# Kernel optimization log

Hardware: AMD Instinct MI355X
Metric: run time of the kernel (lower is better)

## Reference

```python
import jax, jax.numpy as jnp
import numpy as np

B, IN, E, NCLS = 1024, 784, 256, 10
BRAIN, ADIM, NJUMPS = 4, 3, 4
N = BRAIN ** ADIM  # 64 blocks
TAU = 1.0
_GKEY = jax.random.key(42)  # fixed key -> deterministic gumbel noise


def _gumbel_softmax_hard(key, logits):
    u = jax.random.uniform(key, logits.shape, minval=1e-6, maxval=1.0 - 1e-6)
    g = -jnp.log(-jnp.log(u))
    y = jax.nn.softmax((logits + g) / TAU, axis=-1)
    hard = jax.nn.one_hot(jnp.argmax(y, axis=-1), logits.shape[-1], dtype=y.dtype)
    return jax.lax.stop_gradient(hard - y) + y  # straight-through


def _next_address(state, key, at0_W1, at0_b1, at0_W2, at0_b2):
    # always uses block 0's address_transform (as in the original forward)
    h = jax.nn.relu(state @ at0_W1 + at0_b1)
    logits = (h @ at0_W2 + at0_b2).reshape(state.shape[0], ADIM, BRAIN)
    return _gumbel_softmax_hard(key, logits)  # (B, ADIM, BRAIN) one-hot


def _all_blocks(state, st_W1, st_b1, st_W2, st_b2):
    # state: (B,E); st_W*: (N,E,E) stored (in,out). Two batched GEMMs over all N blocks.
    h = jax.nn.relu(jnp.einsum('be,neh->bnh', state, st_W1) + st_b1[None])
    h = jax.nn.relu(jnp.einsum('bnh,nhg->bng', h, st_W2) + st_b2[None])
    norm = jnp.linalg.norm(state, axis=1, keepdims=True)  # (B,1), norm of INPUT state
    return h / (norm[:, :, None] + 1e-6)  # (B,N,E)


def _flatten_onehot(oh):
    # (B, ADIM, BRAIN) -> (B, BRAIN**ADIM) via iterated outer product
    b = oh.shape[0]
    fw = oh[:, 0, :]
    for d in range(1, oh.shape[1]):
        fw = (fw[:, :, None] * oh[:, d, None, :]).reshape(b, -1)
    return fw


def _forward(x, W_emb, b_emb, st_W1, st_b1, st_W2, st_b2,
             at0_W1, at0_b1, at0_W2, at0_b2, out_W1, out_b1, out_W2, out_b2):
    bsz = x.shape[0]
    state = x.reshape(bsz, -1) @ W_emb + b_emb
    initial_state = state
    current_address = _next_address(state, jax.random.fold_in(_GKEY, 0),
                                    at0_W1, at0_b1, at0_W2, at0_b2)
    exited = jnp.zeros((bsz,), dtype=bool)
    exit_states = jnp.zeros_like(state)
    exit_addresses = jnp.zeros_like(current_address)
    for i in range(NJUMPS):  # fixed small jump count; early-break replaced by masking (same math)
        active = ~exited
        bw = _flatten_onehot(current_address)                      # (B,N)
        allout = _all_blocks(state, st_W1, st_b1, st_W2, st_b2)    # (B,N,E)
        new_state = jnp.einsum('bn,bne->be', bw, allout)
        new_address = _next_address(new_state, jax.random.fold_in(_GKEY, i + 1),
                                    at0_W1, at0_b1, at0_W2, at0_b2)
        idx = jnp.argmax(new_address, axis=2)
        is_origin = jnp.all(idx == 0, axis=1) & active
        exit_states = jnp.where(is_origin[:, None], new_state, exit_states)
        exit_addresses = jnp.where(is_origin[:, None, None], new_address, exit_addresses)
        exited = exited | is_origin
        state = jnp.where(active[:, None], new_state, state)
        current_address = jnp.where(active[:, None, None], new_address, current_address)
    final_address = jnp.where(exited[:, None, None], exit_addresses, current_address)
    bw = _flatten_onehot(final_address)
    # original code computes block_out twice and keeps the one using `state` (bug-faithful)
    allout = _all_blocks(state, st_W1, st_b1, st_W2, st_b2)
    final_output = jnp.einsum('bn,bne->be', bw, allout) + initial_state
    h = jax.nn.relu(final_output @ out_W1 + out_b1)
    return h @ out_W2 + out_b2  # (B, NCLS)


def setup_inputs() -> dict:
    key = jax.random.key(0)
    ks = jax.random.split(key, 16)
    s = 0.02
    return {
        'x': jax.random.normal(ks[0], (B, IN), jnp.float32),
        'W_emb': jax.random.normal(ks[1], (IN, E), jnp.float32) * s,
        'b_emb': jnp.zeros((E,), jnp.float32),
        'st_W1': jax.random.normal(ks[2], (N, E, E), jnp.float32) * s,
        'st_b1': jnp.zeros((N, E), jnp.float32),
        'st_W2': jax.random.normal(ks[3], (N, E, E), jnp.float32) * s,
        'st_b2': jnp.zeros((N, E), jnp.float32),
        'at0_W1': jax.random.normal(ks[4], (E, E), jnp.float32) * s,
        'at0_b1': jnp.zeros((E,), jnp.float32),
        'at0_W2': jax.random.normal(ks[5], (E, ADIM * BRAIN), jnp.float32) * s,
        'at0_b2': jnp.zeros((ADIM * BRAIN,), jnp.float32),
        'out_W1': jax.random.normal(ks[6], (E, E), jnp.float32) * s,
        'out_b1': jnp.zeros((E,), jnp.float32),
        'out_W2': jax.random.normal(ks[7], (E, NCLS), jnp.float32) * s,
        'out_b2': jnp.zeros((NCLS,), jnp.float32),
    }


def reference(x, W_emb, b_emb, st_W1, st_b1, st_W2, st_b2,
              at0_W1, at0_b1, at0_W2, at0_b2, out_W1, out_b1, out_W2, out_b2):
    return _forward(x, W_emb, b_emb, st_W1, st_b1, st_W2, st_b2,
                    at0_W1, at0_b1, at0_W2, at0_b2, out_W1, out_b1, out_W2, out_b2)
```

## Files before the change

kernel.cpp:

```cpp
#include <hip/hip_runtime.h>
#include <stdint.h>


#define BATCH 1024
#define EDIM  256
#define INDIM 784
#define GRID_BE 192

__host__ __device__ inline uint32_t rotl32(uint32_t x, uint32_t d) {
  return (x << d) | (x >> (32u - d));
}
__host__ __device__ inline void threefry2x32(uint32_t k0, uint32_t k1,
                                             uint32_t x0, uint32_t x1,
                                             uint32_t* o0, uint32_t* o1) {
  uint32_t ks2 = k0 ^ k1 ^ 0x1BD11BDAu;
  x0 += k0; x1 += k1;
#define TF_R(a) { x0 += x1; x1 = rotl32(x1, a); x1 ^= x0; }
  TF_R(13) TF_R(15) TF_R(26) TF_R(6)   x0 += k1;  x1 += ks2 + 1u;
  TF_R(17) TF_R(29) TF_R(16) TF_R(24)  x0 += ks2; x1 += k0  + 2u;
  TF_R(13) TF_R(15) TF_R(26) TF_R(6)   x0 += k0;  x1 += k1  + 3u;
  TF_R(17) TF_R(29) TF_R(16) TF_R(24)  x0 += k1;  x1 += ks2 + 4u;
  TF_R(13) TF_R(15) TF_R(26) TF_R(6)   x0 += ks2; x1 += k0  + 5u;
#undef TF_R
  *o0 = x0; *o1 = x1;
}
__device__ inline uint32_t jax_bits12288(uint32_t k0, uint32_t k1, uint32_t L) {
  uint32_t o0, o1;
  if (L < 6144u) { threefry2x32(k0, k1, L, L + 6144u, &o0, &o1); return o0; }
  else           { threefry2x32(k0, k1, L - 6144u, L, &o0, &o1); return o1; }
}
__device__ inline float jax_uniform(uint32_t bits) {
  const float minv = 1e-6f;
  const float maxv = (float)(1.0 - 1e-06);
  const float span = maxv - minv;
  uint32_t fb = (bits >> 9) | 0x3f800000u;
  float f = __uint_as_float(fb) - 1.0f;
  float u = __fadd_rn(__fmul_rn(f, span), minv);
  return fmaxf(minv, u);
}

__global__ __launch_bounds__(1024) void k_embed(
    const float* __restrict__ x, const float* __restrict__ Wemb,
    const float* __restrict__ bemb,
    float* __restrict__ stateA, float* __restrict__ initial,
    int* __restrict__ count0) {
  __shared__ float XS[8 * INDIM];
  __shared__ float P[8][128][9];
  const int t = threadIdx.x;
  if (blockIdx.x == 0 && t < 64) count0[t] = 0;
  const int rg = blockIdx.x >> 1, ch = blockIdx.x & 1;
  const int jl = t & 127, ks = t >> 7;

  {
    const float4* src = (const float4*)(x + (size_t)rg * 8 * INDIM);
    float4* dst = (float4*)XS;
    for (int p = t; p < (8 * INDIM) / 4; p += 1024) dst[p] = src[p];
  }
  __syncthreads();

  const int col = ch * 128 + jl;
  const int kb = (ks < 4) ? ks * 100 : 400 + (ks - 4) * 96;
  const int ke = kb + ((ks < 4) ? 100 : 96);
  float a[8] = {0.f,0.f,0.f,0.f,0.f,0.f,0.f,0.f};
#pragma unroll 2
  for (int k = kb; k < ke; k += 4) {
    const float w0 = Wemb[(k+0)*EDIM + col], w1 = Wemb[(k+1)*EDIM + col],
                w2 = Wemb[(k+2)*EDIM + col], w3 = Wemb[(k+3)*EDIM + col];
#pragma unroll
    for (int i = 0; i < 8; i++) {
      const float4 s4 = *(const float4*)&XS[i * INDIM + k];
      a[i] = fmaf(s4.x, w0, a[i]); a[i] = fmaf(s4.y, w1, a[i]);
      a[i] = fmaf(s4.z, w2, a[i]); a[i] = fmaf(s4.w, w3, a[i]);
    }
  }
#pragma unroll
  for (int q = 0; q < 8; q++) P[ks][jl][q] = a[q];
  __syncthreads();
  {
    const int c2 = t & 127, i = t >> 7;
    float s = 0.f;
#pragma unroll
    for (int w = 0; w < 8; w++) s += P[w][c2][i];
    s += bemb[ch * 128 + c2];
    const size_t idx = (size_t)(rg * 8 + i) * EDIM + ch * 128 + c2;
    stateA[idx] = s; initial[idx] = s;
  }
}

__global__ __launch_bounds__(1024) void k_addr(
    const float* __restrict__ state,
    const float* __restrict__ aW1, const float* __restrict__ ab1,
    const float* __restrict__ aW2, const float* __restrict__ ab2,
    int* __restrict__ exited, int* __restrict__ n_next, int* __restrict__ count,
    float* __restrict__ sout, int step, uint32_t fk0, uint32_t fk1) {
  __shared__ float XS[4 * EDIM];
  __shared__ float P[4][256][5];
  __shared__ float H[EDIM][4];
  __shared__ float P2[16][4][16];
  __shared__ float vals[4][12];
  __shared__ int   flags[4];
  const int t = threadIdx.x, b0 = blockIdx.x * 4;

  XS[t] = state[(size_t)b0 * EDIM + t];
  __syncthreads();

  const int j = t & 255, ks = t >> 8;
  const int kb = ks * 64;
  float a[4] = {0.f,0.f,0.f,0.f};
#pragma unroll 2
  for (int k = kb; k < kb + 64; k += 4) {
    const float w0 = aW1[(k+0)*EDIM + j], w1 = aW1[(k+1)*EDIM + j],
                w2 = aW1[(k+2)*EDIM + j], w3 = aW1[(k+3)*EDIM + j];
#pragma unroll
    for (int i = 0; i < 4; i++) {
      const float4 s4 = *(const float4*)&XS[i * EDIM + k];
      a[i] = fmaf(s4.x, w0, a[i]); a[i] = fmaf(s4.y, w1, a[i]);
      a[i] = fmaf(s4.z, w2, a[i]); a[i] = fmaf(s4.w, w3, a[i]);
    }
  }
#pragma unroll
  for (int q = 0; q < 4; q++) P[ks][j][q] = a[q];
  __syncthreads();
  {
    const int j2 = t & 255, i = t >> 8;
    float s = P[0][j2][i] + P[1][j2][i] + P[2][j2][i] + P[3][j2][i] + ab1[j2];
    H[j2][i] = fmaxf(s, 0.f);
  }
  __syncthreads();
  {
    const int c = t & 15, i = (t >> 4) & 3, ksl = t >> 6;
    float a2 = 0.f;
    if (c < 12) {
      const int k0 = ksl * 16;
#pragma unroll 4
      for (int k = k0; k < k0 + 16; k++)
        a2 = fmaf(H[k][i], aW2[k * 12 + c], a2);
    }
    P2[ksl][i][c] = a2;
  }
  __syncthreads();
  if (t < 48) {
    const int i = t / 12, c = t % 12;
    float s = 0.f;
#pragma unroll
    for (int w = 0; w < 16; w++) s += P2[w][i][c];
    const float logit = s + ab2[c];
    const uint32_t L = (uint32_t)((b0 + i) * 12 + c);
    const float u = jax_uniform(jax_bits12288(fk0, fk1, L));
    const float g = -logf(-logf(u));
    vals[i][c] = logit + g;
  }
  __syncthreads();
  if (t < 4) {
    const int b = b0 + t;
    int idx0 = 0, idx1 = 0, idx2 = 0;
    { float best = vals[t][0];
#pragma unroll
      for (int c = 1; c < 4; c++) { float v = vals[t][c];     if (v > best) { best = v; idx0 = c; } } }
    { float best = vals[t][4];
#pragma unroll
      for (int c = 1; c < 4; c++) { float v = vals[t][4 + c]; if (v > best) { best = v; idx1 = c; } } }
    { float best = vals[t][8];
#pragma unroll
      for (int c = 1; c < 4; c++) { float v = vals[t][8 + c]; if (v > best) { best = v; idx2 = c; } } }
    const int nn = idx0 * 16 + idx1 * 4 + idx2;
    int nxt;
    if (step == 0)      { exited[b] = 0; nxt = nn; }
    else if (step < 4)  {
      if (exited[b])      nxt = -1;
      else if (nn == 0) { exited[b] = 1; nxt = -1; }
      else                nxt = nn;
    } else                nxt = exited[b] ? 0 : nn;
    n_next[b] = nxt; flags[t] = nxt;
    if (nxt >= 0) atomicAdd(&count[nxt], 1);
  }
  __syncthreads();
  {
    const int i = t >> 8, jj = t & 255;
    if (flags[i] < 0) sout[(size_t)(b0 + i) * EDIM + jj] = XS[i * EDIM + jj];
  }
}

__global__ __launch_bounds__(1024) void k_blocks(
    const float* __restrict__ sin,
    const float* __restrict__ W1, const float* __restrict__ b1,
    const float* __restrict__ W2, const float* __restrict__ b2,
    const int* __restrict__ count, const int* __restrict__ n_next,
    const float* __restrict__ initial, float* __restrict__ sout,
    int* __restrict__ count_next, int is_final) {
  __shared__ float XS[8 * EDIM];
  __shared__ float P[4][256][9];
  __shared__ float H[EDIM][12];
  __shared__ int   meta[4];
  __shared__ int   rowsl[8];
  __shared__ float denom[8];
  __shared__ int   wcnt[16], wbase[16];
  const int t = threadIdx.x, c = blockIdx.x;
  if (c == 0 && t < 64) count_next[t] = 0;
  if (t < 8) rowsl[t] = 0;
  if (t < 64) {
    const int cnt = count[t];
    const int nch = (cnt + 7) >> 3;
    int icnt = cnt, inch = nch;
#pragma unroll
    for (int d = 1; d < 64; d <<= 1) {
      int t1 = __shfl_up(icnt, d), t2 = __shfl_up(inch, d);
      if (t >= d) { icnt += t1; inch += t2; }
    }
    const int ench = inch - nch;
    const int total = __shfl(inch, 63);
    if (t == 0) meta[3] = total;
    if (c >= ench && c < ench + nch) {
      meta[0] = t; meta[1] = c - ench;
      meta[2] = min(8, cnt - (c - ench) * 8);
    }
  }
  __syncthreads();
  if (c >= meta[3]) return;
  const int n = meta[0], local = meta[1], m = meta[2];

  {
    const bool flag = (n_next[t] == n);
    const unsigned long long bal = __ballot(flag);
    const int wid = t >> 6, lane = t & 63;
    if (lane == 0) wcnt[wid] = __popcll(bal);
    __syncthreads();
    if (t == 0) { int s = 0; for (int w = 0; w < 16; w++) { wbase[w] = s; s += wcnt[w]; } }
    __syncthreads();
    if (flag) {
      const int rank = wbase[wid] + __popcll(bal & ((1ull << lane) - 1ull));
      const int r0 = local * 8;
      if (rank >= r0 && rank < r0 + 8) rowsl[rank - r0] = t;
    }
    __syncthreads();
  }

  if (t < 512) {
    const int i = t >> 6, q = t & 63;
    const int row = rowsl[min(i, m - 1)] & 1023;
    const float4 v = *(const float4*)(sin + (size_t)row * EDIM + q * 4);
    ((float4*)XS)[t] = v;
    float sq = v.x*v.x + v.y*v.y + v.z*v.z + v.w*v.w;
#pragma unroll
    for (int d = 32; d >= 1; d >>= 1) sq += __shfl_xor(sq, d);
    if (q == 0) denom[i] = sqrtf(sq) + 1e-6f;
  }
  __syncthreads();

  const int j = t & 255, ks = t >> 8;
  const int kb = ks * 64;
  const float* W1n = W1 + (size_t)n * EDIM * EDIM;
  {
    float a[8] = {0.f,0.f,0.f,0.f,0.f,0.f,0.f,0.f};
#pragma unroll 2
    for (int k = kb; k < kb + 64; k += 4) {
      const float w0 = W1n[(k+0)*EDIM + j], w1 = W1n[(k+1)*EDIM + j],
                  w2 = W1n[(k+2)*EDIM + j], w3 = W1n[(k+3)*EDIM + j];
#pragma unroll
      for (int i = 0; i < 8; i++) {
        const float4 s4 = *(const float4*)&XS[i * EDIM + k];
        a[i] = fmaf(s4.x, w0, a[i]); a[i] = fmaf(s4.y, w1, a[i]);
        a[i] = fmaf(s4.z, w2, a[i]); a[i] = fmaf(s4.w, w3, a[i]);
      }
    }
#pragma unroll
    for (int q = 0; q < 8; q++) P[ks][j][q] = a[q];
  }
  __syncthreads();
  {
    const int j2 = t & 255, ih = t >> 8;
    const float bb = b1[(size_t)n * EDIM + j2];
#pragma unroll
    for (int qq = 0; qq < 2; qq++) {
      const int i = ih + qq * 4;
      float s = P[0][j2][i] + P[1][j2][i] + P[2][j2][i] + P[3][j2][i] + bb;
      H[j2][i] = fmaxf(s, 0.f);
    }
  }
  __syncthreads();
  const float* W2n = W2 + (size_t)n * EDIM * EDIM;
  {
    float a[8] = {0.f,0.f,0.f,0.f,0.f,0.f,0.f,0.f};
#pragma unroll 4
    for (int k = kb; k < kb + 64; k++) {
      const float w = W2n[k*EDIM + j];
      const float4 h0 = *(const float4*)&H[k][0];
      const float4 h1 = *(const float4*)&H[k][4];
      a[0] = fmaf(h0.x, w, a[0]); a[1] = fmaf(h0.y, w, a[1]);
      a[2] = fmaf(h0.z, w, a[2]); a[3] = fmaf(h0.w, w, a[3]);
      a[4] = fmaf(h1.x, w, a[4]); a[5] = fmaf(h1.y, w, a[5]);
      a[6] = fmaf(h1.z, w, a[6]); a[7] = fmaf(h1.w, w, a[7]);
    }
#pragma unroll
    for (int q = 0; q < 8; q++) P[ks][j][q] = a[q];
  }
  __syncthreads();
  {
    const int col = t & 255, ih = t >> 8;
    const float bb2 = b2[(size_t)n * EDIM + col];
#pragma unroll
    for (int qq = 0; qq < 2; qq++) {
      const int i = ih + qq * 4;
      if (i < m) {
        float s = P[0][col][i] + P[1][col][i] + P[2][col][i] + P[3][col][i] + bb2;
        float v = fmaxf(s, 0.f) / denom[i];
        const int row = rowsl[i] & 1023;
        if (is_final) v += initial[(size_t)row * EDIM + col];
        sout[(size_t)row * EDIM + col] = v;
      }
    }
  }
}

__global__ __launch_bounds__(1024) void k_head(
    const float* __restrict__ fin,
    const float* __restrict__ oW1, const float* __restrict__ ob1,
    const float* __restrict__ oW2, const float* __restrict__ ob2,
    float* __restrict__ out) {
  __shared__ float XS[4 * EDIM];
  __shared__ float P[4][256][5];
  __shared__ float H[EDIM][4];
  __shared__ float P2[16][4][16];
  const int t = threadIdx.x, b0 = blockIdx.x * 4;
  XS[t] = fin[(size_t)b0 * EDIM + t];
  __syncthreads();
  const int j = t & 255, ks = t >> 8;
  const int kb = ks * 64;
  float a[4] = {0.f,0.f,0.f,0.f};
#pragma unroll 2
  for (int k = kb; k < kb + 64; k += 4) {
    const float w0 = oW1[(k+0)*EDIM + j], w1 = oW1[(k+1)*EDIM + j],
                w2 = oW1[(k+2)*EDIM + j], w3 = oW1[(k+3)*EDIM + j];
#pragma unroll
    for (int i = 0; i < 4; i++) {
      const float4 s4 = *(const float4*)&XS[i * EDIM + k];
      a[i] = fmaf(s4.x, w0, a[i]); a[i] = fmaf(s4.y, w1, a[i]);
      a[i] = fmaf(s4.z, w2, a[i]); a[i] = fmaf(s4.w, w3, a[i]);
    }
  }
#pragma unroll
  for (int q = 0; q < 4; q++) P[ks][j][q] = a[q];
  __syncthreads();
  {
    const int j2 = t & 255, i = t >> 8;
    float s = P[0][j2][i] + P[1][j2][i] + P[2][j2][i] + P[3][j2][i] + ob1[j2];
    H[j2][i] = fmaxf(s, 0.f);
  }
  __syncthreads();
  {
    const int c = t & 15, i = (t >> 4) & 3, ksl = t >> 6;
    float a2 = 0.f;
    if (c < 10) {
      const int k0 = ksl * 16;
#pragma unroll 4
      for (int k = k0; k < k0 + 16; k++)
        a2 = fmaf(H[k][i], oW2[k * 10 + c], a2);
    }
    P2[ksl][i][c] = a2;
  }
  __syncthreads();
  if (t < 40) {
    const int i = t / 10, c = t % 10;
    float s = 0.f;
#pragma unroll
    for (int w = 0; w < 16; w++) s += P2[w][i][c];
    out[(size_t)(b0 + i) * 10 + c] = s + ob2[c];
  }
}

extern "C" void kernel_launch(void* const* d_in, const int* in_sizes, int n_in,
                              void* d_out, int out_size, void* d_ws, size_t ws_size,
                              hipStream_t stream) {
  const float* x    = (const float*)d_in[0];
  const float* Wemb = (const float*)d_in[1];
  const float* bemb = (const float*)d_in[2];
  const float* stW1 = (const float*)d_in[3];
  const float* stb1 = (const float*)d_in[4];
  const float* stW2 = (const float*)d_in[5];
  const float* stb2 = (const float*)d_in[6];
  const float* aW1  = (const float*)d_in[7];
  const float* ab1  = (const float*)d_in[8];
  const float* aW2  = (const float*)d_in[9];
  const float* ab2  = (const float*)d_in[10];
  const float* oW1  = (const float*)d_in[11];
  const float* ob1  = (const float*)d_in[12];
  const float* oW2  = (const float*)d_in[13];
  const float* ob2  = (const float*)d_in[14];
  float* out = (float*)d_out;

  char* ws = (char*)d_ws;
  auto alloc = [&](size_t bytes) { char* p = ws; ws += (bytes + 255) & ~(size_t)255; return p; };
  float* stateA  = (float*)alloc((size_t)BATCH * EDIM * 4);
  float* stateB  = (float*)alloc((size_t)BATCH * EDIM * 4);
  float* initial = (float*)alloc((size_t)BATCH * EDIM * 4);
  float* finalb  = (float*)alloc((size_t)BATCH * EDIM * 4);
  int* exited = (int*)alloc(BATCH * 4);
  int* n_next = (int*)alloc(BATCH * 4);
  int* counters[2];
  counters[0] = (int*)alloc(64 * 4);
  counters[1] = (int*)alloc(64 * 4);

  uint32_t fk0[5], fk1[5];
  for (uint32_t s = 0; s < 5; s++) threefry2x32(0u, 42u, 0u, s, &fk0[s], &fk1[s]);

  k_embed<<<256, 1024, 0, stream>>>(x, Wemb, bemb, stateA, initial, counters[0]);

  float* cur = stateA;
  float* nxt = stateB;
  for (int j = 0; j < 5; j++) {
    int* cnt  = counters[j & 1];
    int* cntN = counters[(j + 1) & 1];
    float* dst = (j < 4) ? nxt : finalb;
    k_addr<<<BATCH / 4, 1024, 0, stream>>>(cur, aW1, ab1, aW2, ab2,
        exited, n_next, cnt, dst, j, fk0[j], fk1[j]);
    k_blocks<<<GRID_BE, 1024, 0, stream>>>(cur, stW1, stb1, stW2, stb2,
        cnt, n_next, initial, dst, cntN, (j == 4) ? 1 : 0);
    if (j < 4) { float* tmp = cur; cur = nxt; nxt = tmp; }
  }
  k_head<<<BATCH / 4, 1024, 0, stream>>>(finalb, oW1, ob1, oW2, ob2, out);
}
```

Before: 265.9 us.

## Restructure pipeline: fuse embed with first address, fuse final block with head

Rewrites most kernels. The embedding GEMM and the first address step now run in one kernel, and the last block step runs together with the output head. Kernels drop from 1024 to 256 threads and use a register-tiled 4x4 micro-GEMM. Routing moves to per-step index arrays, replacing the exited/count/double-buffer state, and Gumbel keys are now derived on the device. This cuts launches and global round-trips but changes occupancy and in-place state update semantics, which carries correctness risk.

```diff
diff --git a/kernel.cpp b/kernel.cpp
--- a/kernel.cpp
+++ b/kernel.cpp
@@ -5,7 +5,8 @@
 #define BATCH 1024
 #define EDIM  256
 #define INDIM 784
-#define GRID_BE 192
+#define CH    4
+#define GRID_B 304
 
 __host__ __device__ inline uint32_t rotl32(uint32_t x, uint32_t d) {
   return (x << d) | (x >> (32u - d));
@@ -38,333 +39,488 @@
   float u = __fadd_rn(__fmul_rn(f, span), minv);
   return fmaxf(minv, u);
 }
-
-__global__ __launch_bounds__(1024) void k_embed(
+__device__ inline float gumbel_val(int s, int b, int c) {
+  uint32_t fk0, fk1;
+  threefry2x32(0u, 42u, 0u, (uint32_t)s, &fk0, &fk1);
+  const uint32_t L = (uint32_t)(b * 12 + c);
+  const float u = jax_uniform(jax_bits12288(fk0, fk1, L));
+  return -logf(-logf(u));
+}
+__device__ inline int addr_argmax(const float* v) {
+  int i0 = 0, i1 = 0, i2 = 0;
+  { float b = v[0];
+    for (int c = 1; c < 4; c++) { float x = v[c];     if (x > b) { b = x; i0 = c; } } }
+  { float b = v[4];
+    for (int c = 1; c < 4; c++) { float x = v[4 + c]; if (x > b) { b = x; i1 = c; } } }
+  { float b = v[8];
+    for (int c = 1; c < 4; c++) { float x = v[8 + c]; if (x > b) { b = x; i2 = c; } } }
+  return i0 * 16 + i1 * 4 + i2;
+}
+
+#define GEMM_TILE(Wbase, XSarr, SROW, kb, KS, acc)                              \
+  {                                                                             \
+    const float* Wc = (Wbase) + (size_t)(kb) * EDIM + jc;                       \
+    _Pragma("unroll 1")                                                         \
+    for (int kk = 0; kk < (KS); kk += 4) {                                      \
+      float wv[16];                                                             \
+      _Pragma("unroll")                                                         \
+      for (int q = 0; q < 4; q++) {                                             \
+        _Pragma("unroll")                                                       \
+        for (int cc = 0; cc < 4; cc++)                                          \
+          wv[q * 4 + cc] = Wc[(size_t)(kk + q) * EDIM + cc * 64];               \
+      }                                                                         \
+      const int k = (kb) + kk;                                                  \
+      const float4 r0 = *(const float4*)&(XSarr)[0 * (SROW) + k];               \
+      const float4 r1 = *(const float4*)&(XSarr)[1 * (SROW) + k];               \
+      const float4 r2 = *(const float4*)&(XSarr)[2 * (SROW) + k];               \
+      const float4 r3 = *(const float4*)&(XSarr)[3 * (SROW) + k];               \
+      _Pragma("unroll")                                                         \
+      for (int cc = 0; cc < 4; cc++) {                                          \
+        acc[0][cc] = fmaf(r0.x, wv[0 + cc], acc[0][cc]);                        \
+        acc[0][cc] = fmaf(r0.y, wv[4 + cc], acc[0][cc]);                        \
+        acc[0][cc] = fmaf(r0.z, wv[8 + cc], acc[0][cc]);                        \
+        acc[0][cc] = fmaf(r0.w, wv[12 + cc], acc[0][cc]);                       \
+        acc[1][cc] = fmaf(r1.x, wv[0 + cc], acc[1][cc]);                        \
+        acc[1][cc] = fmaf(r1.y, wv[4 + cc], acc[1][cc]);                        \
+        acc[1][cc] = fmaf(r1.z, wv[8 + cc], acc[1][cc]);                        \
+        acc[1][cc] = fmaf(r1.w, wv[12 + cc], acc[1][cc]);                       \
+        acc[2][cc] = fmaf(r2.x, wv[0 + cc], acc[2][cc]);                        \
+        acc[2][cc] = fmaf(r2.y, wv[4 + cc], acc[2][cc]);                        \
+        acc[2][cc] = fmaf(r2.z, wv[8 + cc], acc[2][cc]);                        \
+        acc[2][cc] = fmaf(r2.w, wv[12 + cc], acc[2][cc]);                       \
+        acc[3][cc] = fmaf(r3.x, wv[0 + cc], acc[3][cc]);                        \
+        acc[3][cc] = fmaf(r3.y, wv[4 + cc], acc[3][cc]);                        \
+        acc[3][cc] = fmaf(r3.z, wv[8 + cc], acc[3][cc]);                        \
+        acc[3][cc] = fmaf(r3.w, wv[12 + cc], acc[3][cc]);                       \
+      }                                                                         \
+    }                                                                           \
+  }
+
+#define P_STORE(P, kg, jc, acc)                                                 \
+  { _Pragma("unroll")                                                           \
+    for (int cc = 0; cc < 4; cc++) {                                            \
+      const int col = (jc) + cc * 64;                                           \
+      *(float4*)&(P)[(((kg) * 256) + col) * 4] =                                \
+        make_float4(acc[0][cc], acc[1][cc], acc[2][cc], acc[3][cc]);            \
+    } }
+
+#define GEMM_TILE_H(Wbase, Harr, kb, KS, acc)                                   \
+  {                                                                             \
+    const float* Wc = (Wbase) + (size_t)(kb) * EDIM + jc;                       \
+    _Pragma("unroll 1")                                                         \
+    for (int kk = 0; kk < (KS); kk += 4) {                                      \
+      float wv[16];                                                             \
+      _Pragma("unroll")                                                         \
+      for (int q = 0; q < 4; q++) {                                             \
+        _Pragma("unroll")                                                       \
+        for (int cc = 0; cc < 4; cc++)                                          \
+          wv[q * 4 + cc] = Wc[(size_t)(kk + q) * EDIM + cc * 64];               \
+      }                                                                         \
+      _Pragma("unroll")                                                         \
+      for (int q = 0; q < 4; q++) {                                             \
+        const float4 h = *(const float4*)&(Harr)[((kb) + kk + q) * 4];          \
+        _Pragma("unroll")                                                       \
+        for (int cc = 0; cc < 4; cc++) {                                        \
+          acc[0][cc] = fmaf(h.x, wv[q * 4 + cc], acc[0][cc]);                   \
+          acc[1][cc] = fmaf(h.y, wv[q * 4 + cc], acc[1][cc]);                   \
+          acc[2][cc] = fmaf(h.z, wv[q * 4 + cc], acc[2][cc]);                   \
+          acc[3][cc] = fmaf(h.w, wv[q * 4 + cc], acc[3][cc]);                   \
+        }                                                                       \
+      }                                                                         \
+    }                                                                           \
+  }
+
+#define ADDR_TAIL(P, H, P2a, vals, ab1, aW2, ab2, astep, b0)                    \
+  {                                                                             \
+    { const int col = t;                                                        \
+      float4 p0 = *(const float4*)&(P)[((0 * 256) + col) * 4];                  \
+      float4 p1 = *(const float4*)&(P)[((1 * 256) + col) * 4];                  \
+      float4 p2 = *(const float4*)&(P)[((2 * 256) + col) * 4];                  \
+      float4 p3 = *(const float4*)&(P)[((3 * 256) + col) * 4];                  \
+      const float bb = (ab1)[col];                                              \
+      *(float4*)&(H)[col * 4] = make_float4(                                    \
+        fmaxf(p0.x + p1.x + p2.x + p3.x + bb, 0.f),                             \
+        fmaxf(p0.y + p1.y + p2.y + p3.y + bb, 0.f),                             \
+        fmaxf(p0.z + p1.z + p2.z + p3.z + bb, 0.f),                             \
+        fmaxf(p0.w + p1.w + p2.w + p3.w + bb, 0.f));                            \
+    }                                                                           \
+    __syncthreads();                                                            \
+    { const int c = t & 15, ksl = t >> 4;                                       \
+      float a2[4] = {0.f, 0.f, 0.f, 0.f};                                       \
+      if (c < 12) {                                                             \
+        const int k0 = ksl * 16;                                                \
+        _Pragma("unroll 4")                                                     \
+        for (int k = k0; k < k0 + 16; k++) {                                    \
+          const float4 h = *(const float4*)&(H)[k * 4];                         \
+          const float w = (aW2)[k * 12 + c];                                    \
+          a2[0] = fmaf(h.x, w, a2[0]); a2[1] = fmaf(h.y, w, a2[1]);             \
+          a2[2] = fmaf(h.z, w, a2[2]); a2[3] = fmaf(h.w, w, a2[3]);             \
+        }                                                                       \
+      }                                                                         \
+      *(float4*)&(P2a)[(ksl * 16 + c) * 4] = make_float4(a2[0], a2[1], a2[2], a2[3]); \
+    }                                                                           \
+    __syncthreads();                                                            \
+    if (t < 48) {                                                               \
+      const int i = t / 12, c = t % 12;                                         \
+      float s = 0.f;                                                            \
+      _Pragma("unroll")                                                         \
+      for (int w = 0; w < 16; w++) s += (P2a)[(w * 16 + c) * 4 + i];            \
+      (vals)[i * 12 + c] = s + (ab2)[c] + gumbel_val((astep), (b0) + i, c);     \
+    }                                                                           \
+    __syncthreads();                                                            \
+  }
+
+__global__ __launch_bounds__(256, 4) void k_embed_a0(
     const float* __restrict__ x, const float* __restrict__ Wemb,
     const float* __restrict__ bemb,
-    float* __restrict__ stateA, float* __restrict__ initial,
-    int* __restrict__ count0) {
-  __shared__ float XS[8 * INDIM];
-  __shared__ float P[8][128][9];
-  const int t = threadIdx.x;
-  if (blockIdx.x == 0 && t < 64) count0[t] = 0;
-  const int rg = blockIdx.x >> 1, ch = blockIdx.x & 1;
-  const int jl = t & 127, ks = t >> 7;
-
-  {
-    const float4* src = (const float4*)(x + (size_t)rg * 8 * INDIM);
-    float4* dst = (float4*)XS;
-    for (int p = t; p < (8 * INDIM) / 4; p += 1024) dst[p] = src[p];
-  }
-  __syncthreads();
-
-  const int col = ch * 128 + jl;
-  const int kb = (ks < 4) ? ks * 100 : 400 + (ks - 4) * 96;
-  const int ke = kb + ((ks < 4) ? 100 : 96);
-  float a[8] = {0.f,0.f,0.f,0.f,0.f,0.f,0.f,0.f};
-#pragma unroll 2
-  for (int k = kb; k < ke; k += 4) {
-    const float w0 = Wemb[(k+0)*EDIM + col], w1 = Wemb[(k+1)*EDIM + col],
-                w2 = Wemb[(k+2)*EDIM + col], w3 = Wemb[(k+3)*EDIM + col];
-#pragma unroll
-    for (int i = 0; i < 8; i++) {
-      const float4 s4 = *(const float4*)&XS[i * INDIM + k];
-      a[i] = fmaf(s4.x, w0, a[i]); a[i] = fmaf(s4.y, w1, a[i]);
-      a[i] = fmaf(s4.z, w2, a[i]); a[i] = fmaf(s4.w, w3, a[i]);
-    }
-  }
-#pragma unroll
-  for (int q = 0; q < 8; q++) P[ks][jl][q] = a[q];
-  __syncthreads();
-  {
-    const int c2 = t & 127, i = t >> 7;
-    float s = 0.f;
-#pragma unroll
-    for (int w = 0; w < 8; w++) s += P[w][c2][i];
-    s += bemb[ch * 128 + c2];
-    const size_t idx = (size_t)(rg * 8 + i) * EDIM + ch * 128 + c2;
-    stateA[idx] = s; initial[idx] = s;
-  }
-}
-
-__global__ __launch_bounds__(1024) void k_addr(
+    const float* __restrict__ aW1, const float* __restrict__ ab1,
+    const float* __restrict__ aW2, const float* __restrict__ ab2,
+    float* __restrict__ state, float* __restrict__ initial,
+    int* __restrict__ nn_all) {
+  __shared__ __align__(16) float XS[4 * INDIM];
+  __shared__ __align__(16) float P[4 * 256 * 4];
+  __shared__ __align__(16) float SS[4 * EDIM];
+  __shared__ __align__(16) float H[EDIM * 4];
+  __shared__ __align__(16) float P2a[16 * 16 * 4];
+  __shared__ float vals[4 * 12];
+  const int t = threadIdx.x, b0 = blockIdx.x * 4;
+  const int jc = t & 63, kg = t >> 6;
+
+  { const float4* src = (const float4*)(x + (size_t)b0 * INDIM);
+    for (int p = t; p < INDIM; p += 256) ((float4*)XS)[p] = src[p];
+  }
+  __syncthreads();
+
+  {
+    const int kb = kg * 196;
+    float acc[4][4] = {};
+    GEMM_TILE(Wemb, XS, INDIM, kb, 196, acc);
+    P_STORE(P, kg, jc, acc);
+  }
+  __syncthreads();
+  {
+    const int col = t;
+    float4 p0 = *(const float4*)&P[((0 * 256) + col) * 4];
+    float4 p1 = *(const float4*)&P[((1 * 256) + col) * 4];
+    float4 p2 = *(const float4*)&P[((2 * 256) + col) * 4];
+    float4 p3 = *(const float4*)&P[((3 * 256) + col) * 4];
+    const float bb = bemb[col];
+    float s0 = p0.x + p1.x + p2.x + p3.x + bb;
+    float s1 = p0.y + p1.y + p2.y + p3.y + bb;
+    float s2 = p0.z + p1.z + p2.z + p3.z + bb;
+    float s3 = p0.w + p1.w + p2.w + p3.w + bb;
+    SS[0 * EDIM + col] = s0; SS[1 * EDIM + col] = s1;
+    SS[2 * EDIM + col] = s2; SS[3 * EDIM + col] = s3;
+    state[(size_t)(b0 + 0) * EDIM + col] = s0; initial[(size_t)(b0 + 0) * EDIM + col] = s0;
+    state[(size_t)(b0 + 1) * EDIM + col] = s1; initial[(size_t)(b0 + 1) * EDIM + col] = s1;
+    state[(size_t)(b0 + 2) * EDIM + col] = s2; initial[(size_t)(b0 + 2) * EDIM + col] = s2;
+    state[(size_t)(b0 + 3) * EDIM + col] = s3; initial[(size_t)(b0 + 3) * EDIM + col] = s3;
+  }
+  __syncthreads();
+
+  {
+    const int kb = kg * 64;
+    float acc[4][4] = {};
+    GEMM_TILE(aW1, SS, EDIM, kb, 64, acc);
+    P_STORE(P, kg, jc, acc);
+  }
+  __syncthreads();
+  ADDR_TAIL(P, H, P2a, vals, ab1, aW2, ab2, 0, b0);
+  if (t < 4) nn_all[b0 + t] = addr_argmax(&vals[t * 12]);
+}
+
+__global__ __launch_bounds__(256, 4) void k_addr(
     const float* __restrict__ state,
     const float* __restrict__ aW1, const float* __restrict__ ab1,
     const float* __restrict__ aW2, const float* __restrict__ ab2,
-    int* __restrict__ exited, int* __restrict__ n_next, int* __restrict__ count,
-    float* __restrict__ sout, int step, uint32_t fk0, uint32_t fk1) {
-  __shared__ float XS[4 * EDIM];
-  __shared__ float P[4][256][5];
-  __shared__ float H[EDIM][4];
-  __shared__ float P2[16][4][16];
-  __shared__ float vals[4][12];
-  __shared__ int   flags[4];
+    const int* __restrict__ nn_prev, int* __restrict__ nn_out, int step) {
+  __shared__ __align__(16) float XS[4 * EDIM];
+  __shared__ __align__(16) float P[4 * 256 * 4];
+  __shared__ __align__(16) float H[EDIM * 4];
+  __shared__ __align__(16) float P2a[16 * 16 * 4];
+  __shared__ float vals[4 * 12];
   const int t = threadIdx.x, b0 = blockIdx.x * 4;
-
-  XS[t] = state[(size_t)b0 * EDIM + t];
-  __syncthreads();
-
-  const int j = t & 255, ks = t >> 8;
-  const int kb = ks * 64;
-  float a[4] = {0.f,0.f,0.f,0.f};
-#pragma unroll 2
-  for (int k = kb; k < kb + 64; k += 4) {
-    const float w0 = aW1[(k+0)*EDIM + j], w1 = aW1[(k+1)*EDIM + j],
-                w2 = aW1[(k+2)*EDIM + j], w3 = aW1[(k+3)*EDIM + j];
-#pragma unroll
-    for (int i = 0; i < 4; i++) {
-      const float4 s4 = *(const float4*)&XS[i * EDIM + k];
-      a[i] = fmaf(s4.x, w0, a[i]); a[i] = fmaf(s4.y, w1, a[i]);
-      a[i] = fmaf(s4.z, w2, a[i]); a[i] = fmaf(s4.w, w3, a[i]);
-    }
-  }
-#pragma unroll
-  for (int q = 0; q < 4; q++) P[ks][j][q] = a[q];
-  __syncthreads();
-  {
-    const int j2 = t & 255, i = t >> 8;
-    float s = P[0][j2][i] + P[1][j2][i] + P[2][j2][i] + P[3][j2][i] + ab1[j2];
-    H[j2][i] = fmaxf(s, 0.f);
-  }
-  __syncthreads();
-  {
-    const int c = t & 15, i = (t >> 4) & 3, ksl = t >> 6;
-    float a2 = 0.f;
-    if (c < 12) {
-      const int k0 = ksl * 16;
-#pragma unroll 4
-      for (int k = k0; k < k0 + 16; k++)
-        a2 = fmaf(H[k][i], aW2[k * 12 + c], a2);
-    }
-    P2[ksl][i][c] = a2;
-  }
-  __syncthreads();
-  if (t < 48) {
-    const int i = t / 12, c = t % 12;
-    float s = 0.f;
-#pragma unroll
-    for (int w = 0; w < 16; w++) s += P2[w][i][c];
-    const float logit = s + ab2[c];
-    const uint32_t L = (uint32_t)((b0 + i) * 12 + c);
-    const float u = jax_uniform(jax_bits12288(fk0, fk1, L));
-    const float g = -logf(-logf(u));
-    vals[i][c] = logit + g;
-  }
-  __syncthreads();
+  const int jc = t & 63, kg = t >> 6;
+
+  ((float4*)XS)[t] = ((const float4*)(state + (size_t)b0 * EDIM))[t];
+  __syncthreads();
+
+  { const int kb = kg * 64;
+    float acc[4][4] = {};
+    GEMM_TILE(aW1, XS, EDIM, kb, 64, acc);
+    P_STORE(P, kg, jc, acc);
+  }
+  __syncthreads();
+  ADDR_TAIL(P, H, P2a, vals, ab1, aW2, ab2, step, b0);
   if (t < 4) {
     const int b = b0 + t;
-    int idx0 = 0, idx1 = 0, idx2 = 0;
-    { float best = vals[t][0];
-#pragma unroll
-      for (int c = 1; c < 4; c++) { float v = vals[t][c];     if (v > best) { best = v; idx0 = c; } } }
-    { float best = vals[t][4];
-#pragma unroll
-      for (int c = 1; c < 4; c++) { float v = vals[t][4 + c]; if (v > best) { best = v; idx1 = c; } } }
-    { float best = vals[t][8];
-#pragma unroll
-      for (int c = 1; c < 4; c++) { float v = vals[t][8 + c]; if (v > best) { best = v; idx2 = c; } } }
-    const int nn = idx0 * 16 + idx1 * 4 + idx2;
     int nxt;
-    if (step == 0)      { exited[b] = 0; nxt = nn; }
-    else if (step < 4)  {
-      if (exited[b])      nxt = -1;
-      else if (nn == 0) { exited[b] = 1; nxt = -1; }
-      else                nxt = nn;
-    } else                nxt = exited[b] ? 0 : nn;
-    n_next[b] = nxt; flags[t] = nxt;
-    if (nxt >= 0) atomicAdd(&count[nxt], 1);
-  }
-  __syncthreads();
-  {
-    const int i = t >> 8, jj = t & 255;
-    if (flags[i] < 0) sout[(size_t)(b0 + i) * EDIM + jj] = XS[i * EDIM + jj];
-  }
-}
-
-__global__ __launch_bounds__(1024) void k_blocks(
-    const float* __restrict__ sin,
+    if (nn_prev[b] < 0) nxt = -1;
+    else {
+      const int nn = addr_argmax(&vals[t * 12]);
+      nxt = (step < 4 && nn == 0) ? -1 : nn;
+    }
+    nn_out[b] = nxt;
+  }
+}
+
+#define B_ROUTE(nnval_expr)                                                     \
+  if (t < 64) hist[t] = 0;                                                      \
+  if (t < 4) rowsl[t] = 0;                                                      \
+  __syncthreads();                                                              \
+  int myv[4]; bool fl[4];                                                       \
+  _Pragma("unroll")                                                             \
+  for (int p = 0; p < 4; p++) {                                                 \
+    const int rr = p * 256 + t;                                                 \
+    myv[p] = (nnval_expr);                                                      \
+    if (myv[p] >= 0) atomicAdd(&hist[myv[p]], 1);                               \
+  }                                                                             \
+  __syncthreads();                                                              \
+  if (t < 64) {                                                                 \
+    const int cnt = hist[t];                                                    \
+    const int nch = (cnt + CH - 1) / CH;                                        \
+    int icnt = cnt, inch = nch;                                                 \
+    _Pragma("unroll")                                                           \
+    for (int d = 1; d < 64; d <<= 1) {                                          \
+      int t1 = __shfl_up(icnt, d), t2 = __shfl_up(inch, d);                     \
+      if (t >= d) { icnt += t1; inch += t2; }                                   \
+    }                                                                           \
+    const int ench = inch - nch;                                                \
+    if (t == 63) meta[3] = inch;                                                \
+    if (c >= ench && c < ench + nch) {                                          \
+      meta[0] = t; meta[1] = c - ench;                                          \
+      meta[2] = min(CH, cnt - (c - ench) * CH);                                 \
+    }                                                                           \
+  }                                                                             \
+  __syncthreads();                                                              \
+  if (c >= meta[3]) return;                                                     \
+  const int n = meta[0], local = meta[1], m = meta[2];                          \
+  {                                                                             \
+    const int wid = t >> 6, lane = t & 63;                                      \
+    unsigned long long bals[4];                                                 \
+    _Pragma("unroll")                                                           \
+    for (int p = 0; p < 4; p++) {                                               \
+      fl[p] = (myv[p] == n);                                                    \
+      bals[p] = __ballot(fl[p]);                                                \
+      if (lane == 0) wcnt2[p * 4 + wid] = __popcll(bals[p]);                    \
+    }                                                                           \
+    __syncthreads();                                                            \
+    if (t == 0) { int s = 0;                                                    \
+      for (int e = 0; e < 16; e++) { wbase2[e] = s; s += wcnt2[e]; } }          \
+    __syncthreads();                                                            \
+    const int r0 = local * CH;                                                  \
+    _Pragma("unroll")                                                           \
+    for (int p = 0; p < 4; p++) {                                               \
+      if (fl[p]) {                                                              \
+        const int rank = wbase2[p * 4 + wid] +                                  \
+          __popcll(bals[p] & ((1ull << lane) - 1ull));                          \
+        if (rank >= r0 && rank < r0 + CH) rowsl[rank - r0] = p * 256 + t;       \
+      }                                                                         \
+    }                                                                           \
+    __syncthreads();                                                            \
+  }
+
+__global__ __launch_bounds__(256, 4) void k_blocks(
+    float* __restrict__ state,
     const float* __restrict__ W1, const float* __restrict__ b1,
     const float* __restrict__ W2, const float* __restrict__ b2,
-    const int* __restrict__ count, const int* __restrict__ n_next,
-    const float* __restrict__ initial, float* __restrict__ sout,
-    int* __restrict__ count_next, int is_final) {
-  __shared__ float XS[8 * EDIM];
-  __shared__ float P[4][256][9];
-  __shared__ float H[EDIM][12];
-  __shared__ int   meta[4];
-  __shared__ int   rowsl[8];
-  __shared__ float denom[8];
-  __shared__ int   wcnt[16], wbase[16];
-  const int t = threadIdx.x, c = blockIdx.x;
-  if (c == 0 && t < 64) count_next[t] = 0;
-  if (t < 8) rowsl[t] = 0;
-  if (t < 64) {
-    const int cnt = count[t];
-    const int nch = (cnt + 7) >> 3;
-    int icnt = cnt, inch = nch;
-#pragma unroll
-    for (int d = 1; d < 64; d <<= 1) {
-      int t1 = __shfl_up(icnt, d), t2 = __shfl_up(inch, d);
-      if (t >= d) { icnt += t1; inch += t2; }
-    }
-    const int ench = inch - nch;
-    const int total = __shfl(inch, 63);
-    if (t == 0) meta[3] = total;
-    if (c >= ench && c < ench + nch) {
-      meta[0] = t; meta[1] = c - ench;
-      meta[2] = min(8, cnt - (c - ench) * 8);
-    }
-  }
-  __syncthreads();
-  if (c >= meta[3]) return;
-  const int n = meta[0], local = meta[1], m = meta[2];
-
-  {
-    const bool flag = (n_next[t] == n);
-    const unsigned long long bal = __ballot(flag);
-    const int wid = t >> 6, lane = t & 63;
-    if (lane == 0) wcnt[wid] = __popcll(bal);
-    __syncthreads();
-    if (t == 0) { int s = 0; for (int w = 0; w < 16; w++) { wbase[w] = s; s += wcnt[w]; } }
-    __syncthreads();
-    if (flag) {
-      const int rank = wbase[wid] + __popcll(bal & ((1ull << lane) - 1ull));
-      const int r0 = local * 8;
-      if (rank >= r0 && rank < r0 + 8) rowsl[rank - r0] = t;
-    }
-    __syncthreads();
-  }
-
-  if (t < 512) {
+    const int* __restrict__ nnj) {
+  __shared__ __align__(16) float XS[4 * EDIM];
+  __shared__ __align__(16) float P[4 * 256 * 4];
+  __shared__ __align__(16) float H[EDIM * 4];
+  __shared__ int hist[64], meta[4], rowsl[4];
+  __shared__ int wcnt2[16], wbase2[16];
+  __shared__ float denom[4];
+  const int t = threadIdx.x;
+  const int c = ((blockIdx.x & 7) * 38) + (blockIdx.x >> 3);
+  const int jc = t & 63, kg = t >> 6;
+
+  B_ROUTE(nnj[rr])
+
+  {
     const int i = t >> 6, q = t & 63;
     const int row = rowsl[min(i, m - 1)] & 1023;
-    const float4 v = *(const float4*)(sin + (size_t)row * EDIM + q * 4);
+    const float4 v = *(const float4*)(state + (size_t)row * EDIM + q * 4);
     ((float4*)XS)[t] = v;
-    float sq = v.x*v.x + v.y*v.y + v.z*v.z + v.w*v.w;
+    float sq = v.x * v.x + v.y * v.y + v.z * v.z + v.w * v.w;
 #pragma unroll
     for (int d = 32; d >= 1; d >>= 1) sq += __shfl_xor(sq, d);
     if (q == 0) denom[i] = sqrtf(sq) + 1e-6f;
   }
   __syncthreads();
 
-  const int j = t & 255, ks = t >> 8;
-  const int kb = ks * 64;
   const float* W1n = W1 + (size_t)n * EDIM * EDIM;
-  {
-    float a[8] = {0.f,0.f,0.f,0.f,0.f,0.f,0.f,0.f};
-#pragma unroll 2
-    for (int k = kb; k < kb + 64; k += 4) {
-      const float w0 = W1n[(k+0)*EDIM + j], w1 = W1n[(k+1)*EDIM + j],
-                  w2 = W1n[(k+2)*EDIM + j], w3 = W1n[(k+3)*EDIM + j];
+  const float* W2n = W2 + (size_t)n * EDIM * EDIM;
+  const int kb = kg * 64;
+  { float acc[4][4] = {};
+    GEMM_TILE(W1n, XS, EDIM, kb, 64, acc);
+    P_STORE(P, kg, jc, acc);
+  }
+  __syncthreads();
+  {
+    const int col = t;
+    float4 p0 = *(const float4*)&P[((0 * 256) + col) * 4];
+    float4 p1 = *(const float4*)&P[((1 * 256) + col) * 4];
+    float4 p2 = *(const float4*)&P[((2 * 256) + col) * 4];
+    float4 p3 = *(const float4*)&P[((3 * 256) + col) * 4];
+    const float bb = b1[(size_t)n * EDIM + col];
+    *(float4*)&H[col * 4] = make_float4(
+      fmaxf(p0.x + p1.x + p2.x + p3.x + bb, 0.f),
+      fmaxf(p0.y + p1.y + p2.y + p3.y + bb, 0.f),
+      fmaxf(p0.z + p1.z + p2.z + p3.z + bb, 0.f),
+      fmaxf(p0.w + p1.w + p2.w + p3.w + bb, 0.f));
+  }
+  __syncthreads();
+  { float acc[4][4] = {};
+    GEMM_TILE_H(W2n, H, kb, 64, acc);
+    P_STORE(P, kg, jc, acc);
+  }
+  __syncthreads();
+  {
+    const int col = t;
+    float4 p0 = *(const float4*)&P[((0 * 256) + col) * 4];
+    float4 p1 = *(const float4*)&P[((1 * 256) + col) * 4];
+    float4 p2 = *(const float4*)&P[((2 * 256) + col) * 4];
+    float4 p3 = *(const float4*)&P[((3 * 256) + col) * 4];
+    const float bb = b2[(size_t)n * EDIM + col];
+    float s[4] = { p0.x + p1.x + p2.x + p3.x + bb,
+                   p0.y + p1.y + p2.y + p3.y + bb,
+                   p0.z + p1.z + p2.z + p3.z + bb,
+                   p0.w + p1.w + p2.w + p3.w + bb };
 #pragma unroll
-      for (int i = 0; i < 8; i++) {
-        const float4 s4 = *(const float4*)&XS[i * EDIM + k];
-        a[i] = fmaf(s4.x, w0, a[i]); a[i] = fmaf(s4.y, w1, a[i]);
-        a[i] = fmaf(s4.z, w2, a[i]); a[i] = fmaf(s4.w, w3, a[i]);
+    for (int i = 0; i < 4; i++) {
+      if (i < m) {
+        const int row = rowsl[i] & 1023;
+        state[(size_t)row * EDIM + col] = fmaxf(s[i], 0.f) / denom[i];
       }
     }
-#pragma unroll
-    for (int q = 0; q < 8; q++) P[ks][j][q] = a[q];
-  }
-  __syncthreads();
-  {
-    const int j2 = t & 255, ih = t >> 8;
-    const float bb = b1[(size_t)n * EDIM + j2];
-#pragma unroll
-    for (int qq = 0; qq < 2; qq++) {
-      const int i = ih + qq * 4;
-      float s = P[0][j2][i] + P[1][j2][i] + P[2][j2][i] + P[3][j2][i] + bb;
-      H[j2][i] = fmaxf(s, 0.f);
-    }
-  }
-  __syncthreads();
-  const float* W2n = W2 + (size_t)n * EDIM * EDIM;
-  {
-    float a[8] = {0.f,0.f,0.f,0.f,0.f,0.f,0.f,0.f};
-#pragma unroll 4
-    for (int k = kb; k < kb + 64; k++) {
-      const float w = W2n[k*EDIM + j];
-      const float4 h0 = *(const float4*)&H[k][0];
-      const float4 h1 = *(const float4*)&H[k][4];
-      a[0] = fmaf(h0.x, w, a[0]); a[1] = fmaf(h0.y, w, a[1]);
-      a[2] = fmaf(h0.z, w, a[2]); a[3] = fmaf(h0.w, w, a[3]);
-      a[4] = fmaf(h1.x, w, a[4]); a[5] = fmaf(h1.y, w, a[5]);
-      a[6] = fmaf(h1.z, w, a[6]); a[7] = fmaf(h1.w, w, a[7]);
-    }
-#pragma unroll
-    for (int q = 0; q < 8; q++) P[ks][j][q] = a[q];
-  }
-  __syncthreads();
-  {
-    const int col = t & 255, ih = t >> 8;
-    const float bb2 = b2[(size_t)n * EDIM + col];
-#pragma unroll
-    for (int qq = 0; qq < 2; qq++) {
-      const int i = ih + qq * 4;
-      if (i < m) {
-        float s = P[0][col][i] + P[1][col][i] + P[2][col][i] + P[3][col][i] + bb2;
-        float v = fmaxf(s, 0.f) / denom[i];
-        const int row = rowsl[i] & 1023;
-        if (is_final) v += initial[(size_t)row * EDIM + col];
-        sout[(size_t)row * EDIM + col] = v;
-      }
-    }
-  }
-}
-
-__global__ __launch_bounds__(1024) void k_head(
-    const float* __restrict__ fin,
+  }
+}
+
+__global__ __launch_bounds__(256, 4) void k_block_final(
+    const float* __restrict__ state,
+    const float* __restrict__ W1, const float* __restrict__ b1,
+    const float* __restrict__ W2, const float* __restrict__ b2,
+    const float* __restrict__ initial,
     const float* __restrict__ oW1, const float* __restrict__ ob1,
     const float* __restrict__ oW2, const float* __restrict__ ob2,
-    float* __restrict__ out) {
-  __shared__ float XS[4 * EDIM];
-  __shared__ float P[4][256][5];
-  __shared__ float H[EDIM][4];
-  __shared__ float P2[16][4][16];
-  const int t = threadIdx.x, b0 = blockIdx.x * 4;
-  XS[t] = fin[(size_t)b0 * EDIM + t];
-  __syncthreads();
-  const int j = t & 255, ks = t >> 8;
-  const int kb = ks * 64;
-  float a[4] = {0.f,0.f,0.f,0.f};
-#pragma unroll 2
-  for (int k = kb; k < kb + 64; k += 4) {
-    const float w0 = oW1[(k+0)*EDIM + j], w1 = oW1[(k+1)*EDIM + j],
-                w2 = oW1[(k+2)*EDIM + j], w3 = oW1[(k+3)*EDIM + j];
+    const int* __restrict__ nn4, float* __restrict__ out) {
+  __shared__ __align__(16) float XS[4 * EDIM];
+  __shared__ __align__(16) float P[4 * 256 * 4];
+  __shared__ __align__(16) float H[EDIM * 4];
+  __shared__ __align__(16) float P2h[8 * 16 * 4];
+  __shared__ int hist[64], meta[4], rowsl[4];
+  __shared__ int wcnt2[16], wbase2[16];
+  __shared__ float denom[4];
+  const int t = threadIdx.x;
+  const int c = ((blockIdx.x & 7) * 38) + (blockIdx.x >> 3);
+  const int jc = t & 63, kg = t >> 6;
+
+  B_ROUTE(max(nn4[rr], 0))
+
+  { const int i = t >> 6, q = t & 63;
+    const int row = rowsl[min(i, m - 1)] & 1023;
+    const float4 v = *(const float4*)(state + (size_t)row * EDIM + q * 4);
+    ((float4*)XS)[t] = v;
+    float sq = v.x * v.x + v.y * v.y + v.z * v.z + v.w * v.w;
+#pragma unroll
+    for (int d = 32; d >= 1; d >>= 1) sq += __shfl_xor(sq, d);
+    if (q == 0) denom[i] = sqrtf(sq) + 1e-6f;
+  }
+  __syncthreads();
+
+  const float* W1n = W1 + (size_t)n * EDIM * EDIM;
+  const float* W2n = W2 + (size_t)n * EDIM * EDIM;
+  const int kb = kg * 64;
+  { float acc[4][4] = {};
+    GEMM_TILE(W1n, XS, EDIM, kb, 64, acc);
+    P_STORE(P, kg, jc, acc);
+  }
+  __syncthreads();
+  { const int col = t;
+    float4 p0 = *(const float4*)&P[((0 * 256) + col) * 4];
+    float4 p1 = *(const float4*)&P[((1 * 256) + col) * 4];
+    float4 p2 = *(const float4*)&P[((2 * 256) + col) * 4];
+    float4 p3 = *(const float4*)&P[((3 * 256) + col) * 4];
+    const float bb = b1[(size_t)n * EDIM + col];
+    *(float4*)&H[col * 4] = make_float4(
+      fmaxf(p0.x + p1.x + p2.x + p3.x + bb, 0.f),
+      fmaxf(p0.y + p1.y + p2.y + p3.y + bb, 0.f),
+      fmaxf(p0.z + p1.z + p2.z + p3.z + bb, 0.f),
+      fmaxf(p0.w + p1.w + p2.w + p3.w + bb, 0.f));
+  }
+  __syncthreads();
+  { float acc[4][4] = {};
+    GEMM_TILE_H(W2n, H, kb, 64, acc);
+    P_STORE(P, kg, jc, acc);
+  }
+  __syncthreads();
+  {
+    const int col = t;
+    float4 p0 = *(const float4*)&P[((0 * 256) + col) * 4];
+    float4 p1 = *(const float4*)&P[((1 * 256) + col) * 4];
+    float4 p2 = *(const float4*)&P[((2 * 256) + col) * 4];
+    float4 p3 = *(const float4*)&P[((3 * 256) + col) * 4];
+    const float bb = b2[(size_t)n * EDIM + col];
+    float s[4] = { p0.x + p1.x + p2.x + p3.x + bb,
+                   p0.y + p1.y + p2.y + p3.y + bb,
+                   p0.z + p1.z + p2.z + p3.z + bb,
+                   p0.w + p1.w + p2.w + p3.w + bb };
 #pragma unroll
     for (int i = 0; i < 4; i++) {
-      const float4 s4 = *(const float4*)&XS[i * EDIM + k];
-      a[i] = fmaf(s4.x, w0, a[i]); a[i] = fmaf(s4.y, w1, a[i]);
-      a[i] = fmaf(s4.z, w2, a[i]); a[i] = fmaf(s4.w, w3, a[i]);
+      const int row = rowsl[i] & 1023;
+      float v = fmaxf(s[i], 0.f) / denom[i];
+      v += initial[(size_t)row * EDIM + col];
+      XS[i * EDIM + col] = v;
     }
   }
+  __syncthreads();
+
+  { float acc[4][4] = {};
+    GEMM_TILE(oW1, XS, EDIM, kb, 64, acc);
+    P_STORE(P, kg, jc, acc);
+  }
+  __syncthreads();
+  { const int col = t;
+    float4 p0 = *(const float4*)&P[((0 * 256) + col) * 4];
+    float4 p1 = *(const float4*)&P[((1 * 256) + col) * 4];
+    float4 p2 = *(const float4*)&P[((2 * 256) + col) * 4];
+    float4 p3 = *(const float4*)&P[((3 * 256) + col) * 4];
+    const float bb = ob1[col];
+    *(float4*)&H[col * 4] = make_float4(
+      fmaxf(p0.x + p1.x + p2.x + p3.x + bb, 0.f),
+      fmaxf(p0.y + p1.y + p2.y + p3.y + bb, 0.f),
+      fmaxf(p0.z + p1.z + p2.z + p3.z + bb, 0.f),
+      fmaxf(p0.w + p1.w + p2.w + p3.w + bb, 0.f));
+  }
+  __syncthreads();
+  {
+    if (t < 128) {
+      const int cc = t & 15, ksl = t >> 4;
+      float a2[4] = {0.f, 0.f, 0.f, 0.f};
+      if (cc < 10) {
+        const int k0 = ksl * 32;
+#pragma unroll 4
+        for (int k = k0; k < k0 + 32; k++) {
+          const float4 h = *(const float4*)&H[k * 4];
+          const float w = oW2[k * 10 + cc];
+          a2[0] = fmaf(h.x, w, a2[0]); a2[1] = fmaf(h.y, w, a2[1]);
+          a2[2] = fmaf(h.z, w, a2[2]); a2[3] = fmaf(h.w, w, a2[3]);
+        }
+      }
+      *(float4*)&P2h[(ksl * 16 + cc) * 4] = make_float4(a2[0], a2[1], a2[2], a2[3]);
+    }
+  }
+  __syncthreads();
+  if (t < 40) {
+    const int i = t / 10, cc = t % 10;
+    if (i < m) {
+      float s = 0.f;
 #pragma unroll
-  for (int q = 0; q < 4; q++) P[ks][j][q] = a[q];
-  __syncthreads();
-  {
-    const int j2 = t & 255, i = t >> 8;
-    float s = P[0][j2][i] + P[1][j2][i] + P[2][j2][i] + P[3][j2][i] + ob1[j2];
-    H[j2][i] = fmaxf(s, 0.f);
-  }
-  __syncthreads();
-  {
-    const int c = t & 15, i = (t >> 4) & 3, ksl = t >> 6;
-    float a2 = 0.f;
-    if (c < 10) {
-      const int k0 = ksl * 16;
-#pragma unroll 4
-      for (int k = k0; k < k0 + 16; k++)
-        a2 = fmaf(H[k][i], oW2[k * 10 + c], a2);
+      for (int w = 0; w < 8; w++) s += P2h[(w * 16 + cc) * 4 + i];
+      const int row = rowsl[i] & 1023;
+      out[(size_t)row * 10 + cc] = s + ob2[cc];
     }
-    P2[ksl][i][c] = a2;
-  }
-  __syncthreads();
-  if (t < 40) {
-    const int i = t / 10, c = t % 10;
-    float s = 0.f;
-#pragma unroll
-    for (int w = 0; w < 16; w++) s += P2[w][i][c];
-    out[(size_t)(b0 + i) * 10 + c] = s + ob2[c];
   }
 }
 
@@ -390,32 +546,20 @@
 
   char* ws = (char*)d_ws;
   auto alloc = [&](size_t bytes) { char* p = ws; ws += (bytes + 255) & ~(size_t)255; return p; };
-  float* stateA  = (float*)alloc((size_t)BATCH * EDIM * 4);
-  float* stateB  = (float*)alloc((size_t)BATCH * EDIM * 4);
+  float* state   = (float*)alloc((size_t)BATCH * EDIM * 4);
   float* initial = (float*)alloc((size_t)BATCH * EDIM * 4);
-  float* finalb  = (float*)alloc((size_t)BATCH * EDIM * 4);
-  int* exited = (int*)alloc(BATCH * 4);
-  int* n_next = (int*)alloc(BATCH * 4);
-  int* counters[2];
-  counters[0] = (int*)alloc(64 * 4);
-  counters[1] = (int*)alloc(64 * 4);
-
-  uint32_t fk0[5], fk1[5];
-  for (uint32_t s = 0; s < 5; s++) threefry2x32(0u, 42u, 0u, s, &fk0[s], &fk1[s]);
-
-  k_embed<<<256, 1024, 0, stream>>>(x, Wemb, bemb, stateA, initial, counters[0]);
-
-  float* cur = stateA;
-  float* nxt = stateB;
-  for (int j = 0; j < 5; j++) {
-    int* cnt  = counters[j & 1];
-    int* cntN = counters[(j + 1) & 1];
-    float* dst = (j < 4) ? nxt : finalb;
-    k_addr<<<BATCH / 4, 1024, 0, stream>>>(cur, aW1, ab1, aW2, ab2,
-        exited, n_next, cnt, dst, j, fk0[j], fk1[j]);
-    k_blocks<<<GRID_BE, 1024, 0, stream>>>(cur, stW1, stb1, stW2, stb2,
-        cnt, n_next, initial, dst, cntN, (j == 4) ? 1 : 0);
-    if (j < 4) { float* tmp = cur; cur = nxt; nxt = tmp; }
-  }
-  k_head<<<BATCH / 4, 1024, 0, stream>>>(finalb, oW1, ob1, oW2, ob2, out);
-}
+  int*   nn_all  = (int*)alloc(5 * BATCH * 4);
+
+  k_embed_a0<<<BATCH / 4, 256, 0, stream>>>(x, Wemb, bemb, aW1, ab1, aW2, ab2,
+                                            state, initial, nn_all);
+  for (int j = 0; j < 4; j++) {
+    k_blocks<<<GRID_B, 256, 0, stream>>>(state, stW1, stb1, stW2, stb2,
+                                         nn_all + j * BATCH);
+    k_addr<<<BATCH / 4, 256, 0, stream>>>(state, aW1, ab1, aW2, ab2,
+                                          nn_all + j * BATCH,
+                                          nn_all + (j + 1) * BATCH, j + 1);
+  }
+  k_block_final<<<GRID_B, 256, 0, stream>>>(state, stW1, stb1, stW2, stb2,
+                                            initial, oW1, ob1, oW2, ob2,
+                                            nn_all + 4 * BATCH, out);
+}
```

New measurement: 255.2 us. 4.0% less time.
